# Kernel tuning notes

Hardware: AMD Instinct MI355X
Metric: run time of the kernel (lower is better)

The kernel has to match this reference:

```python
import jax, jax.numpy as jnp
import numpy as np

HIDDEN = 768
KV_DIM = HIDDEN // 3  # 256
BATCH, SEQ = 2, 8192
THETA = 10000.0


def rope_table(seq_len, dim):
    # Matches LlamaRotaryEmbedding: returns [1, seq_len, dim] sinusoid table
    pos = jnp.arange(seq_len, dtype=jnp.float32)                       # [S]
    freqs = THETA ** (-jnp.arange(0, dim, 2, dtype=jnp.float32) / dim)  # [dim/2]
    ang = pos[:, None] * freqs[None, :]                                 # [S, dim/2]
    return jnp.concatenate([jnp.sin(ang), jnp.cos(ang)], axis=-1)[None]  # [1, S, dim]


def setup_inputs() -> dict:
    key = jax.random.key(0)
    kx, kq, kk, kv, ko = jax.random.split(key, 5)
    s = 1.0 / np.sqrt(HIDDEN)
    return {
        "x": jax.random.normal(kx, (BATCH, SEQ, HIDDEN), dtype=jnp.float32),
        # torch nn.Linear weights: [out_features, in_features], y = x @ W.T
        "Wq": jax.random.uniform(kq, (HIDDEN, HIDDEN), jnp.float32, -s, s),
        "Wk": jax.random.uniform(kk, (KV_DIM, HIDDEN), jnp.float32, -s, s),
        "Wv": jax.random.uniform(kv, (KV_DIM, HIDDEN), jnp.float32, -s, s),
        "Wo": jax.random.uniform(ko, (HIDDEN, KV_DIM), jnp.float32, -s, s),
    }


def reference(x, Wq, Wk, Wv, Wo):
    B, S, H = x.shape
    # q/k projections are computed in the original but immediately OVERWRITTEN
    # by the rope table (the rope module ignores its input values). Kept here
    # for faithfulness; XLA will DCE them in forward.
    q = jnp.einsum('bsh,oh->bso', x, Wq)
    k = jnp.einsum('bsh,oh->bso', x, Wk)
    v = jnp.einsum('bsh,oh->bso', x, Wv)                # [B, S, KV_DIM]
    r = rope_table(S, H)                                 # [1, S, H] -> q == k == r
    attn_weights = jnp.matmul(r, jnp.swapaxes(r, -2, -1))  # [1, S, S]
    attn_probs = jax.nn.softmax(attn_weights, axis=-1)      # [1, S, S]
    attn_output = jnp.matmul(attn_probs, v)                 # broadcast -> [B, S, KV_DIM]
    out = jnp.einsum('bsk,ok->bso', attn_output, Wo)        # [B, S, H]
    return out
```

## Files before the change

kernel.cpp:

```cpp
#include <hip/hip_runtime.h>


typedef unsigned short u16;
typedef __attribute__((ext_vector_type(8))) short short8;
typedef __attribute__((ext_vector_type(8))) _Float16 f16x8;
typedef __attribute__((ext_vector_type(4))) float float4v;

__device__ inline u16 f16b(float f) {
  union { _Float16 h; u16 u; } v; v.h = (_Float16)f; return v.u;
}

__device__ inline u16 f32_to_bf16(float f) {
  union { float f; unsigned int u; } v; v.f = f;
  unsigned int r = v.u + 0x7FFF + ((v.u >> 16) & 1);
  return (u16)(r >> 16);
}

__device__ inline void gld_lds16(const u16* g, u16* l) {
  auto gp = (const __attribute__((address_space(1))) unsigned int*)(g);
  auto lp = (__attribute__((address_space(3))) unsigned int*)(l);
  __builtin_amdgcn_global_load_lds(gp, lp, 16, 0, 0);
}

__global__ __launch_bounds__(256)
void prep_w(const float* __restrict__ Wv, const float* __restrict__ Wo,
            u16* __restrict__ wt) {
  __shared__ __align__(16) float wo[8][256];
  const int og = blockIdx.x / 3, hc = blockIdx.x % 3;
  const int o0 = og * 8;
  {
    const float4v* src = (const float4v*)(Wo + (size_t)o0 * 256);
    float4v* dst = (float4v*)(&wo[0][0]);
    dst[threadIdx.x]       = src[threadIdx.x];
    dst[threadIdx.x + 256] = src[threadIdx.x + 256];
  }
  __syncthreads();
  const int h = hc * 256 + threadIdx.x;
  float acc[8] = {0.f, 0.f, 0.f, 0.f, 0.f, 0.f, 0.f, 0.f};
  for (int k = 0; k < 256; k += 4) {
    float wv0 = Wv[(size_t)(k + 0) * 768 + h];
    float wv1 = Wv[(size_t)(k + 1) * 768 + h];
    float wv2 = Wv[(size_t)(k + 2) * 768 + h];
    float wv3 = Wv[(size_t)(k + 3) * 768 + h];
#pragma unroll
    for (int j = 0; j < 8; ++j) {
      float4v c = *(const float4v*)(&wo[j][k]);
      acc[j] = fmaf(c[0], wv0, acc[j]);
      acc[j] = fmaf(c[1], wv1, acc[j]);
      acc[j] = fmaf(c[2], wv2, acc[j]);
      acc[j] = fmaf(c[3], wv3, acc[j]);
    }
  }
  const int kt = h >> 6, hl = h & 63;
#pragma unroll
  for (int j = 0; j < 8; ++j) {
    const int o = o0 + j;
    wt[((size_t)(kt * 768 + o)) * 64 + (((hl >> 3) ^ (o & 7)) << 3) + (h & 7)] =
        f16b(acc[j]);
  }
}

__global__ __launch_bounds__(512, 4)
void gemm_xw(const float* __restrict__ x, const u16* __restrict__ wt,
             float* __restrict__ out) {
  __shared__ __align__(16) u16 As[2][128 * 64];
  __shared__ __align__(16) u16 Bs[3][128 * 64];
  const int tid = threadIdx.x;
  const int w = tid >> 6, l = tid & 63;
  const int q = l >> 4, mr = l & 15;
  const int wm = w & 1, wn = w >> 1;

  const int sb = (blockIdx.x & 7) * 96 + (blockIdx.x >> 3);
  const int mt = sb / 6, nt = sb - mt * 6;
  const int row0 = mt * 128, col0 = nt * 128;

  const int ar = tid >> 2, ac = (tid & 3) << 4;
  const float* xg = x + (size_t)(row0 + ar) * 768 + ac;
  const int aw0 = ar * 64 + (((ac >> 3) ^ (ar & 7)) << 3);
  const int aw1 = ar * 64 + ((((ac >> 3) + 1) ^ (ar & 7)) << 3);
  const u16* wtb = wt + (size_t)col0 * 64 + tid * 8;

  float4v acc[4][2];
#pragma unroll
  for (int i = 0; i < 4; ++i)
#pragma unroll
    for (int j = 0; j < 2; ++j) acc[i][j] = (float4v){0.f, 0.f, 0.f, 0.f};

  float4v eA0, eA1, eA2, eA3;
  float4v oA0, oA1, oA2, oA3;

#define ISSUE_B(slot, tile)                                                  \
  { const u16* g = wtb + (size_t)(tile) * 49152;                             \
    gld_lds16(g,        &Bs[slot][tid * 8]);                                 \
    gld_lds16(g + 4096, &Bs[slot][4096 + tid * 8]); }

#define ISSUE_A(r0_, r1_, r2_, r3_, tile)                                    \
  { const float* xk = xg + (tile) * 64;                                      \
    r0_ = *(const float4v*)(xk);      r1_ = *(const float4v*)(xk + 4);       \
    r2_ = *(const float4v*)(xk + 8);  r3_ = *(const float4v*)(xk + 12); }

#define CVT_A(r0_, r1_, r2_, r3_, slot)                                      \
  { union { u16 h[8]; short8 s; } p0, p1;                                    \
    _Pragma("unroll")                                                        \
    for (int e = 0; e < 4; ++e) {                                            \
      p0.h[e] = f16b(r0_[e]); p0.h[e + 4] = f16b(r1_[e]);                    \
      p1.h[e] = f16b(r2_[e]); p1.h[e + 4] = f16b(r3_[e]);                    \
    }                                                                        \
    *(short8*)(&As[slot][aw0]) = p0.s;                                       \
    *(short8*)(&As[slot][aw1]) = p1.s; }

#define MFMA_STEP(aslot, bbase)                                              \
  { const u16* Ab = &As[aslot][0];                                           \
    const u16* Bb = (bbase);                                                 \
    __builtin_amdgcn_s_setprio(1);                                           \
    _Pragma("unroll")                                                        \
    for (int kk = 0; kk < 2; ++kk) {                                         \
      f16x8 av[4], bv[2];                                                    \
      _Pragma("unroll")                                                      \
      for (int i = 0; i < 4; ++i) {                                          \
        const int r = wm * 64 + i * 16 + mr;                                 \
        av[i] = *(const f16x8*)(Bb ? &Ab[r * 64 + ((((kk << 2) + q) ^ (r & 7)) << 3)] : 0); \
      }                                                                      \
      _Pragma("unroll")                                                      \
      for (int j = 0; j < 2; ++j) {                                          \
        const int o = wn * 32 + j * 16 + mr;                                 \
        bv[j] = *(const f16x8*)(&Bb[o * 64 + ((((kk << 2) + q) ^ (o & 7)) << 3)]); \
      }                                                                      \
      _Pragma("unroll")                                                      \
      for (int i = 0; i < 4; ++i)                                            \
        _Pragma("unroll")                                                    \
        for (int j = 0; j < 2; ++j)                                          \
          acc[i][j] = __builtin_amdgcn_mfma_f32_16x16x32_f16(av[i], bv[j], acc[i][j], 0, 0, 0); \
    }                                                                        \
    __builtin_amdgcn_s_setprio(0); }

  ISSUE_B(0, 0);
  ISSUE_A(eA0, eA1, eA2, eA3, 0);
  asm volatile("" ::: "memory");
  ISSUE_B(1, 1);
  ISSUE_A(oA0, oA1, oA2, oA3, 1);
  asm volatile("s_waitcnt vmcnt(6)" ::: "memory");
  CVT_A(eA0, eA1, eA2, eA3, 0);
  asm volatile("s_waitcnt lgkmcnt(0)" ::: "memory");
  __builtin_amdgcn_s_barrier();

  int b0 = 0, b1 = 1, b2 = 2;
  for (int p = 0; p < 5; ++p) {
    const int t = 2 * p;
    ISSUE_B(b2, t + 2);
    ISSUE_A(eA0, eA1, eA2, eA3, t + 2);
    asm volatile("s_waitcnt vmcnt(6)" ::: "memory");
    CVT_A(oA0, oA1, oA2, oA3, 1);
    MFMA_STEP(0, &Bs[b0][0]);
    asm volatile("s_waitcnt lgkmcnt(0)" ::: "memory");
    __builtin_amdgcn_s_barrier();
    ISSUE_B(b0, t + 3);
    ISSUE_A(oA0, oA1, oA2, oA3, t + 3);
    asm volatile("s_waitcnt vmcnt(6)" ::: "memory");
    CVT_A(eA0, eA1, eA2, eA3, 0);
    MFMA_STEP(1, &Bs[b1][0]);
    asm volatile("s_waitcnt lgkmcnt(0)" ::: "memory");
    __builtin_amdgcn_s_barrier();
    const int n0 = b2, n1 = b0, n2 = b1;
    b0 = n0; b1 = n1; b2 = n2;
  }

  asm volatile("s_waitcnt vmcnt(0)" ::: "memory");
  CVT_A(oA0, oA1, oA2, oA3, 1);
  MFMA_STEP(0, &Bs[b0][0]);
  asm volatile("s_waitcnt lgkmcnt(0)" ::: "memory");
  __builtin_amdgcn_s_barrier();
  MFMA_STEP(1, &Bs[b1][0]);

#undef ISSUE_B
#undef ISSUE_A
#undef CVT_A
#undef MFMA_STEP

#pragma unroll
  for (int i = 0; i < 4; ++i)
#pragma unroll
    for (int j = 0; j < 2; ++j) {
      const int r0 = row0 + wm * 64 + i * 16 + q * 4;
      const int c  = col0 + wn * 32 + j * 16 + mr;
#pragma unroll
      for (int r = 0; r < 4; ++r)
        out[(size_t)(r0 + r) * 768 + c] = acc[i][j][r];
    }
}

__global__ __launch_bounds__(512, 1)
void fused_fallback(const float* __restrict__ x,
                    const float* __restrict__ Wv, const float* __restrict__ Wo,
                    float* __restrict__ out) {
  __shared__ __align__(16) u16 As[64 * 32];
  __shared__ __align__(16) u16 Bs[256 * 32];
  __shared__ __align__(16) u16 Vs[64 * 264];

  const int tid = threadIdx.x;
  const int w  = tid >> 6, l = tid & 63;
  const int q  = l >> 4, mr = l & 15;
  const int wm = w & 1, wn = w >> 1;
  const int row0 = blockIdx.x * 64;
  const int xr = tid >> 3, xg = (tid & 7) * 4;
  const int wr = tid >> 1, wh = (tid & 1) * 16;

  float4v acc[2][4];
#pragma unroll
  for (int i = 0; i < 2; ++i)
#pragma unroll
    for (int j = 0; j < 4; ++j) acc[i][j] = (float4v){0.f, 0.f, 0.f, 0.f};

  for (int kt = 0; kt < 24; ++kt) {
    const int k0 = kt * 32;
    {
      float4v v = *(const float4v*)(x + (size_t)(row0 + xr) * 768 + k0 + xg);
      union { u16 h[4]; uint2 u; } p;
      p.h[0] = f32_to_bf16(v[0]); p.h[1] = f32_to_bf16(v[1]);
      p.h[2] = f32_to_bf16(v[2]); p.h[3] = f32_to_bf16(v[3]);
      *(uint2*)(As + xr * 32 + xg) = p.u;
    }
    {
      const float* g = Wv + (size_t)wr * 768 + k0 + wh;
      union { u16 h[16]; short8 s[2]; } p;
#pragma unroll
      for (int u = 0; u < 4; ++u) {
        float4v v = *(const float4v*)(g + u * 4);
        p.h[u * 4 + 0] = f32_to_bf16(v[0]); p.h[u * 4 + 1] = f32_to_bf16(v[1]);
        p.h[u * 4 + 2] = f32_to_bf16(v[2]); p.h[u * 4 + 3] = f32_to_bf16(v[3]);
      }
      *(short8*)(Bs + wr * 32 + wh) = p.s[0];
      *(short8*)(Bs + wr * 32 + wh + 8) = p.s[1];
    }
    __syncthreads();

    short8 a[2], b[4];
#pragma unroll
    for (int i = 0; i < 2; ++i)
      a[i] = *(const short8*)(As + (wm * 32 + i * 16 + mr) * 32 + q * 8);
#pragma unroll
    for (int j = 0; j < 4; ++j)
      b[j] = *(const short8*)(Bs + (wn * 64 + j * 16 + mr) * 32 + q * 8);
#pragma unroll
    for (int i = 0; i < 2; ++i)
#pragma unroll
      for (int j = 0; j < 4; ++j)
        acc[i][j] = __builtin_amdgcn_mfma_f32_16x16x32_bf16(a[i], b[j], acc[i][j], 0, 0, 0);
    __syncthreads();
  }

#pragma unroll
  for (int i = 0; i < 2; ++i)
#pragma unroll
    for (int j = 0; j < 4; ++j) {
      int row = wm * 32 + i * 16 + q * 4;
      int col = wn * 64 + j * 16 + mr;
#pragma unroll
      for (int r = 0; r < 4; ++r)
        Vs[(row + r) * 264 + col] = f32_to_bf16(acc[i][j][r]);
    }
  __syncthreads();

  for (int c = 0; c < 3; ++c) {
    float4v acc2[2][4];
#pragma unroll
    for (int i = 0; i < 2; ++i)
#pragma unroll
      for (int j = 0; j < 4; ++j) acc2[i][j] = (float4v){0.f, 0.f, 0.f, 0.f};

    for (int kt = 0; kt < 8; ++kt) {
      const int k0 = kt * 32;
      {
        const float* g = Wo + (size_t)(c * 256 + wr) * 256 + k0 + wh;
        union { u16 h[16]; short8 s[2]; } p;
#pragma unroll
        for (int u = 0; u < 4; ++u) {
          float4v v = *(const float4v*)(g + u * 4);
          p.h[u * 4 + 0] = f32_to_bf16(v[0]); p.h[u * 4 + 1] = f32_to_bf16(v[1]);
          p.h[u * 4 + 2] = f32_to_bf16(v[2]); p.h[u * 4 + 3] = f32_to_bf16(v[3]);
        }
        *(short8*)(Bs + wr * 32 + wh) = p.s[0];
        *(short8*)(Bs + wr * 32 + wh + 8) = p.s[1];
      }
      __syncthreads();

      short8 a[2], b[4];
#pragma unroll
      for (int i = 0; i < 2; ++i)
        a[i] = *(const short8*)(Vs + (wm * 32 + i * 16 + mr) * 264 + k0 + q * 8);
#pragma unroll
      for (int j = 0; j < 4; ++j)
        b[j] = *(const short8*)(Bs + (wn * 64 + j * 16 + mr) * 32 + q * 8);
#pragma unroll
      for (int i = 0; i < 2; ++i)
#pragma unroll
        for (int j = 0; j < 4; ++j)
          acc2[i][j] = __builtin_amdgcn_mfma_f32_16x16x32_bf16(a[i], b[j], acc2[i][j], 0, 0, 0);
      __syncthreads();
    }

#pragma unroll
    for (int i = 0; i < 2; ++i)
#pragma unroll
      for (int j = 0; j < 4; ++j) {
        int row = row0 + wm * 32 + i * 16 + q * 4;
        int col = c * 256 + wn * 64 + j * 16 + mr;
#pragma unroll
        for (int r = 0; r < 4; ++r)
          out[(size_t)(row + r) * 768 + col] = acc2[i][j][r];
      }
  }
}

extern "C" void kernel_launch(void* const* d_in, const int* in_sizes, int n_in,
                              void* d_out, int out_size, void* d_ws, size_t ws_size,
                              hipStream_t stream) {
  (void)in_sizes; (void)n_in; (void)out_size;
  const float* x  = (const float*)d_in[0];
  const float* Wv = (const float*)d_in[3];
  const float* Wo = (const float*)d_in[4];
  float* out = (float*)d_out;

  if (ws_size >= (size_t)768 * 768 * 2) {
    u16* wt = (u16*)d_ws;
    prep_w<<<dim3(288), dim3(256), 0, stream>>>(Wv, Wo, wt);
    gemm_xw<<<dim3(768), dim3(512), 0, stream>>>(x, wt, out);
  } else {
    fused_fallback<<<dim3(256), dim3(512), 0, stream>>>(x, Wv, Wo, out);
  }
}
```

Baseline: 151.9 us.

## Halve K-tile to 32, use 4-warp blocks with 64x64 warp tiles

The GEMM block shrinks from 512 to 256 threads. Each warp now computes a 64x64 tile with a 4x4 MFMA accumulator grid, and the K-tile drops from 64 to 32 with a new 2-bit swizzle, giving more pipeline iterations. Weight prep now handles 4 output rows per block over twice as many blocks and writes the new 32-wide layout. The goal is fewer LDS fragment reads per MFMA and smaller LDS use, at the cost of more accumulator registers and more barrier steps.

```diff
diff --git a/kernel.cpp b/kernel.cpp
--- a/kernel.cpp
+++ b/kernel.cpp
@@ -22,49 +22,52 @@
   __builtin_amdgcn_global_load_lds(gp, lp, 16, 0, 0);
 }
 
+__device__ inline int swzkey(int r) { return ((r >> 1) ^ (r >> 3)) & 3; }
+
 __global__ __launch_bounds__(256)
 void prep_w(const float* __restrict__ Wv, const float* __restrict__ Wo,
             u16* __restrict__ wt) {
-  __shared__ __align__(16) float wo[8][256];
+  __shared__ __align__(16) float wo[4][256];
   const int og = blockIdx.x / 3, hc = blockIdx.x % 3;
-  const int o0 = og * 8;
-  {
-    const float4v* src = (const float4v*)(Wo + (size_t)o0 * 256);
-    float4v* dst = (float4v*)(&wo[0][0]);
-    dst[threadIdx.x]       = src[threadIdx.x];
-    dst[threadIdx.x + 256] = src[threadIdx.x + 256];
-  }
+  const int o0 = og * 4;
+  ((float4v*)&wo[0][0])[threadIdx.x] =
+      ((const float4v*)(Wo + (size_t)o0 * 256))[threadIdx.x];
   __syncthreads();
   const int h = hc * 256 + threadIdx.x;
-  float acc[8] = {0.f, 0.f, 0.f, 0.f, 0.f, 0.f, 0.f, 0.f};
-  for (int k = 0; k < 256; k += 4) {
-    float wv0 = Wv[(size_t)(k + 0) * 768 + h];
-    float wv1 = Wv[(size_t)(k + 1) * 768 + h];
-    float wv2 = Wv[(size_t)(k + 2) * 768 + h];
-    float wv3 = Wv[(size_t)(k + 3) * 768 + h];
-#pragma unroll
-    for (int j = 0; j < 8; ++j) {
-      float4v c = *(const float4v*)(&wo[j][k]);
-      acc[j] = fmaf(c[0], wv0, acc[j]);
-      acc[j] = fmaf(c[1], wv1, acc[j]);
-      acc[j] = fmaf(c[2], wv2, acc[j]);
-      acc[j] = fmaf(c[3], wv3, acc[j]);
-    }
-  }
-  const int kt = h >> 6, hl = h & 63;
-#pragma unroll
-  for (int j = 0; j < 8; ++j) {
+  float acc[4] = {0.f, 0.f, 0.f, 0.f};
+  for (int k = 0; k < 256; k += 8) {
+    float wv[8];
+#pragma unroll
+    for (int u = 0; u < 8; ++u) wv[u] = Wv[(size_t)(k + u) * 768 + h];
+#pragma unroll
+    for (int j = 0; j < 4; ++j) {
+      float4v c0 = *(const float4v*)(&wo[j][k]);
+      float4v c1 = *(const float4v*)(&wo[j][k + 4]);
+      acc[j] = fmaf(c0[0], wv[0], acc[j]);
+      acc[j] = fmaf(c0[1], wv[1], acc[j]);
+      acc[j] = fmaf(c0[2], wv[2], acc[j]);
+      acc[j] = fmaf(c0[3], wv[3], acc[j]);
+      acc[j] = fmaf(c1[0], wv[4], acc[j]);
+      acc[j] = fmaf(c1[1], wv[5], acc[j]);
+      acc[j] = fmaf(c1[2], wv[6], acc[j]);
+      acc[j] = fmaf(c1[3], wv[7], acc[j]);
+    }
+  }
+  const int kt = h >> 5, c = (h >> 3) & 3, kr = h & 7;
+#pragma unroll
+  for (int j = 0; j < 4; ++j) {
     const int o = o0 + j;
-    wt[((size_t)(kt * 768 + o)) * 64 + (((hl >> 3) ^ (o & 7)) << 3) + (h & 7)] =
+    wt[((size_t)(kt * 768 + o)) * 32 + ((c ^ swzkey(o)) << 3) + kr] =
         f16b(acc[j]);
   }
 }
 
-__global__ __launch_bounds__(512, 4)
+__global__ __launch_bounds__(256, 3)
 void gemm_xw(const float* __restrict__ x, const u16* __restrict__ wt,
              float* __restrict__ out) {
-  __shared__ __align__(16) u16 As[2][128 * 64];
-  __shared__ __align__(16) u16 Bs[3][128 * 64];
+  __shared__ __align__(16) u16 As[2][128 * 32];
+  __shared__ __align__(16) u16 Bs[3][128 * 32];
+
   const int tid = threadIdx.x;
   const int w = tid >> 6, l = tid & 63;
   const int q = l >> 4, mr = l & 15;
@@ -74,28 +77,38 @@
   const int mt = sb / 6, nt = sb - mt * 6;
   const int row0 = mt * 128, col0 = nt * 128;
 
-  const int ar = tid >> 2, ac = (tid & 3) << 4;
+  const int ar = tid >> 1, ac = (tid & 1) << 4;
   const float* xg = x + (size_t)(row0 + ar) * 768 + ac;
-  const int aw0 = ar * 64 + (((ac >> 3) ^ (ar & 7)) << 3);
-  const int aw1 = ar * 64 + ((((ac >> 3) + 1) ^ (ar & 7)) << 3);
-  const u16* wtb = wt + (size_t)col0 * 64 + tid * 8;
-
-  float4v acc[4][2];
+  const int fa = swzkey(ar);
+  const int aw0 = ar * 32 + ((((ac >> 3) + 0) ^ fa) << 3);
+  const int aw1 = ar * 32 + ((((ac >> 3) + 1) ^ fa) << 3);
+  const u16* wtb = wt + (size_t)col0 * 32 + tid * 8;
+
+  int avo[4], bvo[4];
+#pragma unroll
+  for (int i = 0; i < 4; ++i) {
+    const int r = wm * 64 + i * 16 + mr;
+    avo[i] = r * 32 + ((q ^ swzkey(r)) << 3);
+    const int o = wn * 64 + i * 16 + mr;
+    bvo[i] = o * 32 + ((q ^ swzkey(o)) << 3);
+  }
+
+  float4v acc[4][4];
 #pragma unroll
   for (int i = 0; i < 4; ++i)
 #pragma unroll
-    for (int j = 0; j < 2; ++j) acc[i][j] = (float4v){0.f, 0.f, 0.f, 0.f};
+    for (int j = 0; j < 4; ++j) acc[i][j] = (float4v){0.f, 0.f, 0.f, 0.f};
 
   float4v eA0, eA1, eA2, eA3;
   float4v oA0, oA1, oA2, oA3;
 
 #define ISSUE_B(slot, tile)                                                  \
-  { const u16* g = wtb + (size_t)(tile) * 49152;                             \
+  { const u16* g = wtb + (size_t)(tile) * 24576;                             \
     gld_lds16(g,        &Bs[slot][tid * 8]);                                 \
-    gld_lds16(g + 4096, &Bs[slot][4096 + tid * 8]); }
+    gld_lds16(g + 2048, &Bs[slot][2048 + tid * 8]); }
 
 #define ISSUE_A(r0_, r1_, r2_, r3_, tile)                                    \
-  { const float* xk = xg + (tile) * 64;                                      \
+  { const float* xk = xg + (size_t)(tile) * 32;                              \
     r0_ = *(const float4v*)(xk);      r1_ = *(const float4v*)(xk + 4);       \
     r2_ = *(const float4v*)(xk + 8);  r3_ = *(const float4v*)(xk + 12); }
 
@@ -112,26 +125,17 @@
 #define MFMA_STEP(aslot, bbase)                                              \
   { const u16* Ab = &As[aslot][0];                                           \
     const u16* Bb = (bbase);                                                 \
+    f16x8 av[4], bv[4];                                                      \
+    _Pragma("unroll")                                                        \
+    for (int i = 0; i < 4; ++i) av[i] = *(const f16x8*)(&Ab[avo[i]]);        \
+    _Pragma("unroll")                                                        \
+    for (int j = 0; j < 4; ++j) bv[j] = *(const f16x8*)(&Bb[bvo[j]]);        \
     __builtin_amdgcn_s_setprio(1);                                           \
     _Pragma("unroll")                                                        \
-    for (int kk = 0; kk < 2; ++kk) {                                         \
-      f16x8 av[4], bv[2];                                                    \
+    for (int i = 0; i < 4; ++i)                                              \
       _Pragma("unroll")                                                      \
-      for (int i = 0; i < 4; ++i) {                                          \
-        const int r = wm * 64 + i * 16 + mr;                                 \
-        av[i] = *(const f16x8*)(Bb ? &Ab[r * 64 + ((((kk << 2) + q) ^ (r & 7)) << 3)] : 0); \
-      }                                                                      \
-      _Pragma("unroll")                                                      \
-      for (int j = 0; j < 2; ++j) {                                          \
-        const int o = wn * 32 + j * 16 + mr;                                 \
-        bv[j] = *(const f16x8*)(&Bb[o * 64 + ((((kk << 2) + q) ^ (o & 7)) << 3)]); \
-      }                                                                      \
-      _Pragma("unroll")                                                      \
-      for (int i = 0; i < 4; ++i)                                            \
-        _Pragma("unroll")                                                    \
-        for (int j = 0; j < 2; ++j)                                          \
-          acc[i][j] = __builtin_amdgcn_mfma_f32_16x16x32_f16(av[i], bv[j], acc[i][j], 0, 0, 0); \
-    }                                                                        \
+      for (int j = 0; j < 4; ++j)                                            \
+        acc[i][j] = __builtin_amdgcn_mfma_f32_16x16x32_f16(av[i], bv[j], acc[i][j], 0, 0, 0); \
     __builtin_amdgcn_s_setprio(0); }
 
   ISSUE_B(0, 0);
@@ -145,7 +149,7 @@
   __builtin_amdgcn_s_barrier();
 
   int b0 = 0, b1 = 1, b2 = 2;
-  for (int p = 0; p < 5; ++p) {
+  for (int p = 0; p < 11; ++p) {
     const int t = 2 * p;
     ISSUE_B(b2, t + 2);
     ISSUE_A(eA0, eA1, eA2, eA3, t + 2);
@@ -180,9 +184,9 @@
 #pragma unroll
   for (int i = 0; i < 4; ++i)
 #pragma unroll
-    for (int j = 0; j < 2; ++j) {
+    for (int j = 0; j < 4; ++j) {
       const int r0 = row0 + wm * 64 + i * 16 + q * 4;
-      const int c  = col0 + wn * 32 + j * 16 + mr;
+      const int c  = col0 + wn * 64 + j * 16 + mr;
 #pragma unroll
       for (int r = 0; r < 4; ++r)
         out[(size_t)(r0 + r) * 768 + c] = acc[i][j][r];
@@ -323,8 +327,8 @@
 
   if (ws_size >= (size_t)768 * 768 * 2) {
     u16* wt = (u16*)d_ws;
-    prep_w<<<dim3(288), dim3(256), 0, stream>>>(Wv, Wo, wt);
-    gemm_xw<<<dim3(768), dim3(512), 0, stream>>>(x, wt, out);
+    prep_w<<<dim3(576), dim3(256), 0, stream>>>(Wv, Wo, wt);
+    gemm_xw<<<dim3(768), dim3(256), 0, stream>>>(x, wt, out);
   } else {
     fused_fallback<<<dim3(256), dim3(512), 0, stream>>>(x, Wv, Wo, out);
   }
```

After: 149.1 us. About the same (-1.8%).
